# Performance work log

Measured on AMD Instinct MI355X. Metric: run time of the kernel, lower is better.

The kernel has to match this reference:

```python
import jax, jax.numpy as jnp
import numpy as np

N = 100000      # nodes
E = 1600000     # edges
F_IN = 64       # num_node_features
R = 8           # num_relations
G = 256         # graphs in batch
H, C = 4, 32    # GAT heads, per-head channels
NEG_SLOPE_ATT = 0.2    # GATConv attention leaky relu
NEG_SLOPE = 0.01       # F.leaky_relu default


def setup_inputs() -> dict:
    key = jax.random.key(0)
    ks = jax.random.split(key, 12)
    init = lambda k, shape, fan: (jax.random.normal(k, shape, jnp.float32) / np.sqrt(fan).astype(np.float32))
    x = jax.random.normal(ks[0], (N, F_IN), jnp.float32)
    edge_index = jax.random.randint(ks[1], (2, E), 0, N)
    edge_type = jax.random.randint(ks[2], (E,), 0, R)
    batch = (jnp.arange(N) * G) // N  # sorted graph ids, every segment non-empty
    return dict(
        x=x, edge_index=edge_index, edge_type=edge_type, batch=batch,
        gat_w=init(ks[3], (F_IN, H * C), F_IN),
        gat_att_src=init(ks[4], (H, C), C),
        gat_att_dst=init(ks[5], (H, C), C),
        gat_bias=jnp.zeros((H * C,), jnp.float32),
        dense1_w=init(ks[6], (H * C, 16), H * C),
        dense1_b=jnp.zeros((16,), jnp.float32),
        rw1=init(ks[7], (R, F_IN, 32), F_IN),
        root1=init(ks[8], (F_IN, 32), F_IN),
        rb1=jnp.zeros((32,), jnp.float32),
        rw2=init(ks[9], (R, 32, 16), 32),
        root2=init(ks[10], (32, 16), 32),
        rb2=jnp.zeros((16,), jnp.float32),
        dense_w=init(ks[11], (32, 1), 32),
        dense_b=jnp.zeros((1,), jnp.float32),
    )


def _gat(x, src, dst, w, att_src, att_dst, bias):
    h = (x @ w).reshape(N, H, C)                       # [N,H,C]
    a_src = jnp.sum(h * att_src, axis=-1)              # [N,H]
    a_dst = jnp.sum(h * att_dst, axis=-1)              # [N,H]
    e = jax.nn.leaky_relu(a_src[src] + a_dst[dst], NEG_SLOPE_ATT)  # [E,H]
    # segment softmax over incoming edges of each dst node
    m = jax.ops.segment_max(e, dst, num_segments=N)    # [N,H]
    p = jnp.exp(e - m[dst])
    s = jax.ops.segment_sum(p, dst, num_segments=N)    # [N,H]
    alpha = p / s[dst]
    msg = h[src] * alpha[:, :, None]                   # [E,H,C]
    out = jax.ops.segment_sum(msg, dst, num_segments=N)
    return out.reshape(N, H * C) + bias


def _rgcn(x, src, dst, edge_type, w, root, bias):
    # per-relation transform of all nodes, then edge gather (PyG RGCNConv, aggr='mean')
    xw = jnp.einsum('ni,rio->rno', x, w)               # [R,N,out]
    msg = xw[edge_type, src]                           # [E,out]
    comb = dst * R + edge_type                         # mean is per (dst, relation)
    cnt = jax.ops.segment_sum(jnp.ones((E,), x.dtype), comb, num_segments=N * R)
    agg = jax.ops.segment_sum(msg / cnt[comb][:, None], dst, num_segments=N)
    return agg + x @ root + bias


def reference(x, edge_index, edge_type, batch, gat_w, gat_att_src, gat_att_dst,
              gat_bias, dense1_w, dense1_b, rw1, root1, rb1, rw2, root2, rb2,
              dense_w, dense_b):
    src, dst = edge_index[0], edge_index[1]
    # GAT branch (dropout treated as identity / eval mode)
    h = _gat(x, src, dst, gat_w, gat_att_src, gat_att_dst, gat_bias)
    h = jax.nn.leaky_relu(h, NEG_SLOPE)
    h = jax.nn.leaky_relu(h @ dense1_w + dense1_b, NEG_SLOPE)
    gmax = jax.ops.segment_max(h, batch, num_segments=G)          # [G,16]
    # RGCN branch
    z = jax.nn.relu(_rgcn(x, src, dst, edge_type, rw1, root1, rb1))
    z = jax.nn.relu(_rgcn(z, src, dst, edge_type, rw2, root2, rb2))
    nodes_per_graph = jax.ops.segment_sum(jnp.ones((N,), x.dtype), batch, num_segments=G)
    gmean = jax.ops.segment_sum(z, batch, num_segments=G) / nodes_per_graph[:, None]
    # fuse
    zc = jnp.concatenate([gmax, gmean], axis=1)                   # [G,32]
    return zc @ dense_w + dense_b                                  # [G,1]
```

## Files before the change

### kernel.cpp

```cpp
#include <hip/hip_runtime.h>
#include <hip/hip_bf16.h>

typedef __hip_bfloat16 bf16;
typedef unsigned short u16;

#define N_NODES 100000
#define N_EDGES 1600000
#define F_IN 64
#define N_REL 8
#define N_GRAPH 256
#define N_HEAD 4
#define HC 128
#define NBLK_SCAN 391

__device__ __forceinline__ float lrelu(float x, float s) { return x >= 0.f ? x : s * x; }
__device__ __forceinline__ unsigned fenc(float f) {
  unsigned b = __float_as_uint(f);
  return (b & 0x80000000u) ? ~b : (b | 0x80000000u);
}
__device__ __forceinline__ float fdec(unsigned u) {
  float v = __uint_as_float((u & 0x80000000u) ? (u & 0x7fffffffu) : ~u);
  return fmaxf(fminf(v, 3e38f), -3e38f);
}
__device__ __forceinline__ float bf2f(bf16 v) { return __bfloat162float(v); }
__device__ __forceinline__ bf16 f2bf(float v) { return __float2bfloat16(v); }
__device__ __forceinline__ float lo_bf(unsigned u) { return __uint_as_float(u << 16); }
__device__ __forceinline__ float hi_bf(unsigned u) { return __uint_as_float(u & 0xFFFF0000u); }
__device__ __forceinline__ unsigned f2bfu(float v) {
  unsigned u = __float_as_uint(v);
  return (u + 0x7FFFu + ((u >> 16) & 1u)) >> 16;
}

template<bool BF> __device__ __forceinline__ float ldf(const void* p, size_t i) {
  if (BF) { u16 v = ((const u16*)p)[i]; return __uint_as_float(((unsigned)v) << 16); }
  else    { return ((const float*)p)[i]; }
}
template<bool BF> __device__ __forceinline__ float2 ldf2(const void* p, size_t i) {
  if (BF) { unsigned v = ((const unsigned*)p)[i]; return make_float2(lo_bf(v), hi_bf(v)); }
  else    { return ((const float2*)p)[i]; }
}

__global__ void k_probe(const u16* __restrict__ xr, int* __restrict__ flag) {
  int t = threadIdx.x;
  int c = 0;
  for (int i = t; i < 1024; i += 256) {
    unsigned e = (xr[i] >> 7) & 0xFFu;
    if (e >= 100u && e <= 140u) c++;
  }
  __shared__ int sc[256];
  sc[t] = c;
  __syncthreads();
  for (int s = 128; s; s >>= 1) { if (t < s) sc[t] += sc[t + s]; __syncthreads(); }
  if (t == 0) *flag = (sc[0] >= 800) ? 1 : 0;
}

template<bool BF>
__device__ __forceinline__ void gat_body(const void* x, const void* w, const void* att_s,
                                         const void* att_d, u16* __restrict__ h,
                                         float* __restrict__ a_src, float* __restrict__ a_dst,
                                         int n0, float* xs) {
  int tid = threadIdx.x;
  for (int i = tid; i < 16 * F_IN; i += 256)
    xs[i] = ldf<BF>(x, (size_t)(n0 + (i >> 6)) * F_IN + (i & 63));
  __syncthreads();
  int g = tid >> 7, c = tid & 127;
  float as_c = ldf<BF>(att_s, c), ad_c = ldf<BF>(att_d, c);
  float acc[8] = {0.f, 0.f, 0.f, 0.f, 0.f, 0.f, 0.f, 0.f};
#pragma unroll 1
  for (int kh = 0; kh < F_IN; kh += 32) {
    float wreg[32];
#pragma unroll
    for (int j = 0; j < 32; ++j) wreg[j] = ldf<BF>(w, (size_t)(kh + j) * HC + c);
#pragma unroll
    for (int n = 0; n < 8; ++n) {
      const float* xr = &xs[(g * 8 + n) * F_IN + kh];
#pragma unroll
      for (int j = 0; j < 32; j += 4) {
        float4 xv = *(const float4*)&xr[j];
        acc[n] += xv.x * wreg[j];
        acc[n] += xv.y * wreg[j + 1];
        acc[n] += xv.z * wreg[j + 2];
        acc[n] += xv.w * wreg[j + 3];
      }
    }
  }
  int l = tid & 63, head = c >> 5;
#pragma unroll
  for (int n = 0; n < 8; ++n) {
    int node = n0 + g * 8 + n;
    h[(size_t)node * HC + c] = (u16)f2bfu(acc[n]);
    float ps = acc[n] * as_c, pd = acc[n] * ad_c;
#pragma unroll
    for (int off = 16; off > 0; off >>= 1) {
      ps += __shfl_xor(ps, off, 64);
      pd += __shfl_xor(pd, off, 64);
    }
    if ((l & 31) == 0) {
      a_src[node * N_HEAD + head] = ps;
      a_dst[node * N_HEAD + head] = pd;
    }
  }
}

template<bool BF>
__device__ __forceinline__ void xw1_body(const void* x, const void* rw1, bf16* __restrict__ xw1,
                                         int n0, float* xs) {
  int tid = threadIdx.x;
  for (int i = tid; i < 16 * F_IN; i += 256)
    xs[i] = ldf<BF>(x, (size_t)(n0 + (i >> 6)) * F_IN + (i & 63));
  __syncthreads();
  int r = tid >> 5, c = tid & 31;
  float acc[16] = {0.f, 0.f, 0.f, 0.f, 0.f, 0.f, 0.f, 0.f,
                   0.f, 0.f, 0.f, 0.f, 0.f, 0.f, 0.f, 0.f};
#pragma unroll 1
  for (int kh = 0; kh < F_IN; kh += 32) {
    float wreg[32];
#pragma unroll
    for (int j = 0; j < 32; ++j)
      wreg[j] = ldf<BF>(rw1, (size_t)(r * F_IN + kh + j) * 32 + c);
#pragma unroll
    for (int n = 0; n < 16; ++n) {
      const float* xr = &xs[n * F_IN + kh];
#pragma unroll
      for (int j = 0; j < 32; j += 4) {
        float4 xv = *(const float4*)&xr[j];
        acc[n] += xv.x * wreg[j];
        acc[n] += xv.y * wreg[j + 1];
        acc[n] += xv.z * wreg[j + 2];
        acc[n] += xv.w * wreg[j + 3];
      }
    }
  }
#pragma unroll
  for (int n = 0; n < 16; ++n)
    xw1[((size_t)r * N_NODES + (n0 + n)) * 32 + c] = f2bf(acc[n]);
}

__global__ void __launch_bounds__(256, 4)
k_gxh(const void* x, const void* w, const void* att_s, const void* att_d,
      u16* h, float* a_src, float* a_dst, const void* rw1, bf16* xw1,
      const int* __restrict__ ei, const int* __restrict__ etype,
      int* __restrict__ deg, int* __restrict__ cnt, const int* flag) {
  __shared__ __align__(16) float xs[16 * F_IN];
  int bid = blockIdx.x;
  if (bid < 6250) {
    int e = bid * 256 + threadIdx.x;
    int d = ei[N_EDGES + e], t = etype[e];
    atomicAdd(&deg[d], 1);
    atomicAdd(&cnt[d * N_REL + t], 1);
  } else if (bid < 12500) {
    int n0 = (bid - 6250) * 16;
    if (__builtin_amdgcn_readfirstlane(*flag))
      gat_body<true>(x, w, att_s, att_d, h, a_src, a_dst, n0, xs);
    else
      gat_body<false>(x, w, att_s, att_d, h, a_src, a_dst, n0, xs);
  } else {
    int n0 = (bid - 12500) * 16;
    if (__builtin_amdgcn_readfirstlane(*flag)) xw1_body<true>(x, rw1, xw1, n0, xs);
    else xw1_body<false>(x, rw1, xw1, n0, xs);
  }
}

__global__ void k_scan_a(const int* __restrict__ deg, int* __restrict__ rowptr,
                         int* __restrict__ scanblk) {
  __shared__ int buf[256];
  int tid = threadIdx.x;
  int i = blockIdx.x * 256 + tid;
  int v = (i < N_NODES) ? deg[i] : 0;
  buf[tid] = v;
  __syncthreads();
  for (int st = 1; st < 256; st <<= 1) {
    int t = buf[tid];
    int a = (tid >= st) ? buf[tid - st] : 0;
    __syncthreads();
    buf[tid] = t + a;
    __syncthreads();
  }
  if (i < N_NODES) rowptr[i] = buf[tid] - v;
  if (tid == 255) scanblk[blockIdx.x] = buf[255];
}
__global__ void k_scan_b(int* __restrict__ scanblk) {
  __shared__ int buf[512];
  int tid = threadIdx.x;
  int v = (tid < NBLK_SCAN) ? scanblk[tid] : 0;
  buf[tid] = v;
  __syncthreads();
  for (int st = 1; st < 512; st <<= 1) {
    int t = buf[tid];
    int a = (tid >= st) ? buf[tid - st] : 0;
    __syncthreads();
    buf[tid] = t + a;
    __syncthreads();
  }
  if (tid < NBLK_SCAN) scanblk[tid] = buf[tid] - v;
}
__global__ void k_scan_c(int* __restrict__ rowptr, int* __restrict__ wp,
                         const int* __restrict__ scanblk) {
  int i = blockIdx.x * 256 + threadIdx.x;
  if (i < N_NODES) {
    int val = rowptr[i] + scanblk[blockIdx.x];
    rowptr[i] = val;
    wp[i] = val;
  } else if (i == N_NODES) {
    rowptr[N_NODES] = N_EDGES;
  }
}

__global__ void k_scatter(const int* __restrict__ ei, const int* __restrict__ etype,
                          const float* __restrict__ a_src, const float* __restrict__ a_dst,
                          int* __restrict__ wp, unsigned* __restrict__ csr,
                          float4* __restrict__ p_logit) {
  int e = blockIdx.x * 256 + threadIdx.x;
  if (e >= N_EDGES) return;
  int sn = ei[e], d = ei[N_EDGES + e], t = etype[e];
  int pos = atomicAdd(&wp[d], 1);
  csr[pos] = (unsigned)sn | ((unsigned)t << 20);
  const float4 as = *(const float4*)&a_src[sn * 4];
  const float4 ad = *(const float4*)&a_dst[d * 4];
  float4 lg;
  lg.x = lrelu(as.x + ad.x, 0.2f);
  lg.y = lrelu(as.y + ad.y, 0.2f);
  lg.z = lrelu(as.z + ad.z, 0.2f);
  lg.w = lrelu(as.w + ad.w, 0.2f);
  p_logit[pos] = lg;
}

template<bool BF>
__device__ __forceinline__ void agg_body(const int* __restrict__ rowptr,
                                         const unsigned* __restrict__ csr,
                                         const float* __restrict__ plog,
                                         const uint2* __restrict__ hu2, const void* gbias,
                                         const void* d1w, const void* d1b,
                                         const int* __restrict__ batch,
                                         unsigned* __restrict__ gmax, int* __restrict__ npg,
                                         float (*os)[132], int bid) {
  int tid = threadIdx.x;
  int wave = tid >> 6, l = tid & 63;
  int d = bid * 4 + wave;
  int base = rowptr[d];
  int deg = rowptr[d + 1] - base;
  float m = -1e30f, si;
  {
    int hd = l & 3, sl = l >> 2;
    for (int i = sl; i < deg; i += 16) m = fmaxf(m, plog[(size_t)(base + i) * 4 + hd]);
    m = fmaxf(m, __shfl_xor(m, 4, 64));
    m = fmaxf(m, __shfl_xor(m, 8, 64));
    m = fmaxf(m, __shfl_xor(m, 16, 64));
    m = fmaxf(m, __shfl_xor(m, 32, 64));
    float s = 0.f;
    for (int i = sl; i < deg; i += 16) s += __expf(plog[(size_t)(base + i) * 4 + hd] - m);
    s += __shfl_xor(s, 4, 64);
    s += __shfl_xor(s, 8, 64);
    s += __shfl_xor(s, 16, 64);
    s += __shfl_xor(s, 32, 64);
    si = (deg > 0) ? 1.f / s : 0.f;
  }
  int slot = l >> 5, cl = l & 31;
  int head = cl >> 3;
  float mh = __shfl(m, head, 64);
  float sih = __shfl(si, head, 64);
  float a0 = 0.f, a1 = 0.f, a2 = 0.f, a3 = 0.f;
  int i = slot;
  for (; i + 6 < deg; i += 8) {
    unsigned sp0 = csr[base + i],     sp1 = csr[base + i + 2];
    unsigned sp2 = csr[base + i + 4], sp3 = csr[base + i + 6];
    float av0 = __expf(plog[(size_t)(base + i) * 4 + head] - mh) * sih;
    float av1 = __expf(plog[(size_t)(base + i + 2) * 4 + head] - mh) * sih;
    float av2 = __expf(plog[(size_t)(base + i + 4) * 4 + head] - mh) * sih;
    float av3 = __expf(plog[(size_t)(base + i + 6) * 4 + head] - mh) * sih;
    uint2 h0 = hu2[(size_t)(sp0 & 0xFFFFF) * 32 + cl];
    uint2 h1 = hu2[(size_t)(sp1 & 0xFFFFF) * 32 + cl];
    uint2 h2 = hu2[(size_t)(sp2 & 0xFFFFF) * 32 + cl];
    uint2 h3 = hu2[(size_t)(sp3 & 0xFFFFF) * 32 + cl];
    a0 += lo_bf(h0.x) * av0 + lo_bf(h1.x) * av1 + lo_bf(h2.x) * av2 + lo_bf(h3.x) * av3;
    a1 += hi_bf(h0.x) * av0 + hi_bf(h1.x) * av1 + hi_bf(h2.x) * av2 + hi_bf(h3.x) * av3;
    a2 += lo_bf(h0.y) * av0 + lo_bf(h1.y) * av1 + lo_bf(h2.y) * av2 + lo_bf(h3.y) * av3;
    a3 += hi_bf(h0.y) * av0 + hi_bf(h1.y) * av1 + hi_bf(h2.y) * av2 + hi_bf(h3.y) * av3;
  }
  for (; i < deg; i += 2) {
    unsigned sp = csr[base + i];
    float av = __expf(plog[(size_t)(base + i) * 4 + head] - mh) * sih;
    uint2 hv = hu2[(size_t)(sp & 0xFFFFF) * 32 + cl];
    a0 += lo_bf(hv.x) * av;
    a1 += hi_bf(hv.x) * av;
    a2 += lo_bf(hv.y) * av;
    a3 += hi_bf(hv.y) * av;
  }
  a0 += __shfl_xor(a0, 32, 64);
  a1 += __shfl_xor(a1, 32, 64);
  a2 += __shfl_xor(a2, 32, 64);
  a3 += __shfl_xor(a3, 32, 64);
  if (slot == 0) {
    os[wave][4 * cl + 0] = lrelu(a0 + ldf<BF>(gbias, 4 * cl + 0), 0.01f);
    os[wave][4 * cl + 1] = lrelu(a1 + ldf<BF>(gbias, 4 * cl + 1), 0.01f);
    os[wave][4 * cl + 2] = lrelu(a2 + ldf<BF>(gbias, 4 * cl + 2), 0.01f);
    os[wave][4 * cl + 3] = lrelu(a3 + ldf<BF>(gbias, 4 * cl + 3), 0.01f);
  }
  __syncthreads();
  if (tid < 64) {
    int node = tid >> 4, out = tid & 15;
    float acc = ldf<BF>(d1b, out);
#pragma unroll
    for (int k = 0; k < HC; ++k) acc += os[node][k] * ldf<BF>(d1w, (size_t)k * 16 + out);
    acc = lrelu(acc, 0.01f);
    atomicMax(&gmax[batch[bid * 4 + node] * 16 + out], fenc(acc));
  }
  if (tid < 4) atomicAdd(&npg[batch[bid * 4 + tid]], 1);
}

template<bool BF>
__device__ __forceinline__ void ragg1_body(const int* __restrict__ rowptr,
                                           const unsigned* __restrict__ csr,
                                           const int* __restrict__ cnt,
                                           const unsigned* __restrict__ xw, const void* x,
                                           const void* root1, const void* rb1,
                                           float* __restrict__ z1, float* sh, int bid) {
  float (*xs)[F_IN] = (float(*)[F_IN])sh;
  float (*cinv)[N_REL] = (float(*)[N_REL])(sh + 4 * F_IN);
  int tid = threadIdx.x;
  int n0 = bid * 4;
  {
    int nn = n0 + (tid >> 6);
    xs[tid >> 6][tid & 63] = ldf<BF>(x, (size_t)nn * F_IN + (tid & 63));
  }
  if (tid < 32) {
    int cv = cnt[(n0 + (tid >> 3)) * N_REL + (tid & 7)];
    cinv[tid >> 3][tid & 7] = (cv > 0) ? 1.f / (float)cv : 0.f;
  }
  __syncthreads();
  int wave = tid >> 6, l = tid & 63;
  int slot = l >> 4, cl = l & 15;
  int n = n0 + wave;
  int base = rowptr[n], deg = rowptr[n + 1] - base;
  float a0 = 0.f, a1 = 0.f;
  int i = slot;
  for (; i + 4 < deg; i += 8) {
    unsigned sp0 = csr[base + i], sp1 = csr[base + i + 4];
    int t0 = sp0 >> 20, t1 = sp1 >> 20;
    unsigned v0 = xw[((size_t)t0 * N_NODES + (sp0 & 0xFFFFF)) * 16 + cl];
    unsigned v1 = xw[((size_t)t1 * N_NODES + (sp1 & 0xFFFFF)) * 16 + cl];
    float c0 = cinv[wave][t0], c1 = cinv[wave][t1];
    a0 += lo_bf(v0) * c0 + lo_bf(v1) * c1;
    a1 += hi_bf(v0) * c0 + hi_bf(v1) * c1;
  }
  if (i < deg) {
    unsigned sp = csr[base + i];
    int t = sp >> 20;
    unsigned v = xw[((size_t)t * N_NODES + (sp & 0xFFFFF)) * 16 + cl];
    float c0 = cinv[wave][t];
    a0 += lo_bf(v) * c0;
    a1 += hi_bf(v) * c0;
  }
#pragma unroll
  for (int kk = 0; kk < 16; ++kk) {
    int k = slot * 16 + kk;
    float xv = xs[wave][k];
    float2 wv = ldf2<BF>(root1, (size_t)k * 16 + cl);
    a0 += xv * wv.x;
    a1 += xv * wv.y;
  }
  a0 += __shfl_xor(a0, 16, 64); a0 += __shfl_xor(a0, 32, 64);
  a1 += __shfl_xor(a1, 16, 64); a1 += __shfl_xor(a1, 32, 64);
  if (slot == 0) {
    z1[(size_t)n * 32 + 2 * cl]     = fmaxf(a0 + ldf<BF>(rb1, 2 * cl), 0.f);
    z1[(size_t)n * 32 + 2 * cl + 1] = fmaxf(a1 + ldf<BF>(rb1, 2 * cl + 1), 0.f);
  }
}

__global__ void k_aggragg1(const int* rowptr, const unsigned* csr, const float* plog,
                           const u16* h, const void* gbias, const void* d1w, const void* d1b,
                           const int* batch, unsigned* gmax, int* npg,
                           const int* cnt, const bf16* xw1, const void* x,
                           const void* root1, const void* rb1, float* z1, const int* flag) {
  __shared__ __align__(16) float sh[544];
  int bf = __builtin_amdgcn_readfirstlane(*flag);
  if (blockIdx.x < 25000) {
    if (bf) agg_body<true>(rowptr, csr, plog, (const uint2*)h, gbias, d1w, d1b,
                           batch, gmax, npg, (float(*)[132])sh, blockIdx.x);
    else    agg_body<false>(rowptr, csr, plog, (const uint2*)h, gbias, d1w, d1b,
                            batch, gmax, npg, (float(*)[132])sh, blockIdx.x);
  } else {
    if (bf) ragg1_body<true>(rowptr, csr, cnt, (const unsigned*)xw1, x, root1, rb1, z1,
                             sh, blockIdx.x - 25000);
    else    ragg1_body<false>(rowptr, csr, cnt, (const unsigned*)xw1, x, root1, rb1, z1,
                              sh, blockIdx.x - 25000);
  }
}

template<bool BF>
__device__ __forceinline__ void zw2_body(const float* __restrict__ z1, const void* rw2,
                                         bf16* __restrict__ zw2) {
  __shared__ float zs[16][32];
  int tid = threadIdx.x;
  int n0 = blockIdx.x * 16;
  for (int i = tid; i < 16 * 32; i += 256) {
    int nn = n0 + (i >> 5);
    zs[i >> 5][i & 31] = (nn < N_NODES) ? z1[(size_t)nn * 32 + (i & 31)] : 0.f;
  }
  __syncthreads();
  int nl = tid >> 4, c = tid & 15;
  int n = n0 + nl, r = blockIdx.y;
  float acc = 0.f;
#pragma unroll
  for (int k = 0; k < 32; ++k) acc += zs[nl][k] * ldf<BF>(rw2, (size_t)(r * 32 + k) * 16 + c);
  if (n < N_NODES) zw2[((size_t)r * N_NODES + n) * 16 + c] = f2bf(acc);
}
__global__ void k_zw2(const float* z1, const void* rw2, bf16* zw2, const int* flag) {
  if (__builtin_amdgcn_readfirstlane(*flag)) zw2_body<true>(z1, rw2, zw2);
  else zw2_body<false>(z1, rw2, zw2);
}

template<bool BF>
__device__ __forceinline__ void ragg2_body(const int* __restrict__ rowptr,
                                           const unsigned* __restrict__ csr,
                                           const int* __restrict__ cnt,
                                           const unsigned* __restrict__ zw,
                                           const float* __restrict__ z1, const void* root2,
                                           const void* rb2, const int* __restrict__ batch,
                                           float* __restrict__ gsum) {
  __shared__ float zs[4][33];
  __shared__ float cinv[4][N_REL];
  int tid = threadIdx.x;
  int n0 = blockIdx.x * 4;
  if (tid < 128) {
    int nn = n0 + (tid >> 5);
    zs[tid >> 5][tid & 31] = z1[(size_t)nn * 32 + (tid & 31)];
  }
  if (tid < 32) {
    int cv = cnt[(n0 + (tid >> 3)) * N_REL + (tid & 7)];
    cinv[tid >> 3][tid & 7] = (cv > 0) ? 1.f / (float)cv : 0.f;
  }
  __syncthreads();
  int wave = tid >> 6, l = tid & 63;
  int slot = l >> 3, cl = l & 7;
  int n = n0 + wave;
  int base = rowptr[n], deg = rowptr[n + 1] - base;
  float a0 = 0.f, a1 = 0.f;
  int i = slot;
  for (; i + 8 < deg; i += 16) {
    unsigned sp0 = csr[base + i], sp1 = csr[base + i + 8];
    int t0 = sp0 >> 20, t1 = sp1 >> 20;
    unsigned v0 = zw[((size_t)t0 * N_NODES + (sp0 & 0xFFFFF)) * 8 + cl];
    unsigned v1 = zw[((size_t)t1 * N_NODES + (sp1 & 0xFFFFF)) * 8 + cl];
    float c0 = cinv[wave][t0], c1 = cinv[wave][t1];
    a0 += lo_bf(v0) * c0 + lo_bf(v1) * c1;
    a1 += hi_bf(v0) * c0 + hi_bf(v1) * c1;
  }
  if (i < deg) {
    unsigned sp = csr[base + i];
    int t = sp >> 20;
    unsigned v = zw[((size_t)t * N_NODES + (sp & 0xFFFFF)) * 8 + cl];
    float c0 = cinv[wave][t];
    a0 += lo_bf(v) * c0;
    a1 += hi_bf(v) * c0;
  }
#pragma unroll
  for (int kk = 0; kk < 4; ++kk) {
    int k = slot * 4 + kk;
    float zv = zs[wave][k];
    float2 wv = ldf2<BF>(root2, (size_t)k * 8 + cl);
    a0 += zv * wv.x;
    a1 += zv * wv.y;
  }
  a0 += __shfl_xor(a0, 8, 64); a0 += __shfl_xor(a0, 16, 64); a0 += __shfl_xor(a0, 32, 64);
  a1 += __shfl_xor(a1, 8, 64); a1 += __shfl_xor(a1, 16, 64); a1 += __shfl_xor(a1, 32, 64);
  if (slot == 0) {
    float z2a = fmaxf(a0 + ldf<BF>(rb2, 2 * cl), 0.f);
    float z2b = fmaxf(a1 + ldf<BF>(rb2, 2 * cl + 1), 0.f);
    int g = batch[n];
    atomicAdd(&gsum[g * 16 + 2 * cl], z2a);
    atomicAdd(&gsum[g * 16 + 2 * cl + 1], z2b);
  }
}
__global__ void k_ragg2(const int* rowptr, const unsigned* csr, const int* cnt,
                        const bf16* zw2, const float* z1, const void* root2, const void* rb2,
                        const int* batch, float* gsum, const int* flag) {
  if (__builtin_amdgcn_readfirstlane(*flag))
    ragg2_body<true>(rowptr, csr, cnt, (const unsigned*)zw2, z1, root2, rb2, batch, gsum);
  else
    ragg2_body<false>(rowptr, csr, cnt, (const unsigned*)zw2, z1, root2, rb2, batch, gsum);
}

template<bool BF>
__device__ __forceinline__ void final_body(const unsigned* __restrict__ gmax,
                                           const float* __restrict__ gsum,
                                           const int* __restrict__ npg, const void* dw,
                                           const void* db, void* out) {
  int g = threadIdx.x;
  if (g >= N_GRAPH) return;
  float acc = ldf<BF>(db, 0);
  int np = npg[g]; if (np < 1) np = 1;
  float inv = 1.f / (float)np;
#pragma unroll
  for (int c = 0; c < 16; ++c) {
    acc += fdec(gmax[g * 16 + c]) * ldf<BF>(dw, c);
    acc += (gsum[g * 16 + c] * inv) * ldf<BF>(dw, 16 + c);
  }
  if (BF) ((bf16*)out)[g] = f2bf(acc);
  else ((float*)out)[g] = acc;
}
__global__ void k_final(const unsigned* gmax, const float* gsum, const int* npg,
                        const void* dw, const void* db, void* out, const int* flag) {
  if (__builtin_amdgcn_readfirstlane(*flag)) final_body<true>(gmax, gsum, npg, dw, db, out);
  else final_body<false>(gmax, gsum, npg, dw, db, out);
}

extern "C" void kernel_launch(void* const* d_in, const int* in_sizes, int n_in,
                              void* d_out, int out_size, void* d_ws, size_t ws_size,
                              hipStream_t stream) {
  const void* x        = d_in[0];
  const int*  ei       = (const int*)d_in[1];
  const int*  etype    = (const int*)d_in[2];
  const int*  batch    = (const int*)d_in[3];
  const void* gat_w    = d_in[4];
  const void* att_src  = d_in[5];
  const void* att_dst  = d_in[6];
  const void* gat_bias = d_in[7];
  const void* d1w      = d_in[8];
  const void* d1b      = d_in[9];
  const void* rw1      = d_in[10];
  const void* root1    = d_in[11];
  const void* rb1      = d_in[12];
  const void* rw2      = d_in[13];
  const void* root2    = d_in[14];
  const void* rb2      = d_in[15];
  const void* dw       = d_in[16];
  const void* db       = d_in[17];

  char* ws = (char*)d_ws;
  const size_t o_h     = 0;
  const size_t o_plog  = 25600000;
  const size_t o_xw1   = 51200000;
  const size_t o_zw2   = 0;
  const size_t o_asrc  = 102400000;
  const size_t o_adst  = 104000000;
  const size_t o_deg   = 105600000;
  const size_t o_rowp  = 106000000;
  const size_t o_wp    = 106400016;
  const size_t o_cnt   = 106800016;
  const size_t o_csr   = 110000016;
  const size_t o_z1    = 116400016;
  const size_t o_sblk  = 129200016;
  const size_t o_gmax  = 129201600;
  const size_t o_gsum  = 129217984;
  const size_t o_npg   = 129234368;
  const size_t o_flag  = 129235392;
  const size_t total   = 129235396;
  if (ws_size < total) return;

  u16*      h      = (u16*)(ws + o_h);
  float*    plog   = (float*)(ws + o_plog);
  bf16*     xw1    = (bf16*)(ws + o_xw1);
  bf16*     zw2    = (bf16*)(ws + o_zw2);
  float*    a_src  = (float*)(ws + o_asrc);
  float*    a_dst  = (float*)(ws + o_adst);
  int*      deg    = (int*)(ws + o_deg);
  int*      rowptr = (int*)(ws + o_rowp);
  int*      wp     = (int*)(ws + o_wp);
  int*      cnt    = (int*)(ws + o_cnt);
  unsigned* csr    = (unsigned*)(ws + o_csr);
  float*    z1     = (float*)(ws + o_z1);
  int*      sblk   = (int*)(ws + o_sblk);
  unsigned* gmax   = (unsigned*)(ws + o_gmax);
  float*    gsum   = (float*)(ws + o_gsum);
  int*      npg    = (int*)(ws + o_npg);
  int*      flag   = (int*)(ws + o_flag);

  k_probe<<<1, 256, 0, stream>>>((const u16*)x, flag);

  hipMemsetAsync(ws + o_deg, 0, o_csr - o_deg, stream);
  hipMemsetAsync(ws + o_gmax, 0, 33792, stream);

  k_gxh<<<18750, 256, 0, stream>>>(x, gat_w, att_src, att_dst, h, a_src, a_dst,
                                   rw1, xw1, ei, etype, deg, cnt, flag);

  k_scan_a<<<NBLK_SCAN, 256, 0, stream>>>(deg, rowptr, sblk);
  k_scan_b<<<1, 512, 0, stream>>>(sblk);
  k_scan_c<<<NBLK_SCAN, 256, 0, stream>>>(rowptr, wp, sblk);
  k_scatter<<<(N_EDGES + 255) / 256, 256, 0, stream>>>(ei, etype, a_src, a_dst, wp, csr,
                                                       (float4*)plog);

  k_aggragg1<<<50000, 256, 0, stream>>>(rowptr, csr, plog, h, gat_bias, d1w, d1b,
                                        batch, gmax, npg, cnt, xw1, x, root1, rb1, z1, flag);

  k_zw2<<<dim3((N_NODES + 15) / 16, N_REL), 256, 0, stream>>>(z1, rw2, zw2, flag);
  k_ragg2<<<N_NODES / 4, 256, 0, stream>>>(rowptr, csr, cnt, zw2, z1, root2, rb2,
                                           batch, gsum, flag);

  k_final<<<1, 256, 0, stream>>>(gmax, gsum, npg, dw, db, d_out, flag);
}
```

Measured before the change: 1.085 ms.

## Recompute attention logits in aggregation and fuse z1·rw2 transform into ragg1

The scatter kernel no longer writes a per-edge logit array. The GAT aggregation instead recomputes leaky_relu(a_src[src]+a_dst[dst]) from the CSR, caching up to 128 logits per node in shared memory. The separate zw2 kernel is folded into the RGCN layer-1 aggregation, which computes the per-relation projection from z1 held in shared memory. This removes a 25.6MB logit write and read plus one kernel launch, at the cost of extra gathers of a_src and more shared memory and registers in the fused kernel, now under launch bounds.

```diff
diff --git a/kernel.cpp b/kernel.cpp
--- a/kernel.cpp
+++ b/kernel.cpp
@@ -12,6 +12,7 @@
 #define N_HEAD 4
 #define HC 128
 #define NBLK_SCAN 391
+#define LGCAP 128
 
 __device__ __forceinline__ float lrelu(float x, float s) { return x >= 0.f ? x : s * x; }
 __device__ __forceinline__ unsigned fenc(float f) {
@@ -207,33 +208,23 @@
 }
 
 __global__ void k_scatter(const int* __restrict__ ei, const int* __restrict__ etype,
-                          const float* __restrict__ a_src, const float* __restrict__ a_dst,
-                          int* __restrict__ wp, unsigned* __restrict__ csr,
-                          float4* __restrict__ p_logit) {
+                          int* __restrict__ wp, unsigned* __restrict__ csr) {
   int e = blockIdx.x * 256 + threadIdx.x;
-  if (e >= N_EDGES) return;
   int sn = ei[e], d = ei[N_EDGES + e], t = etype[e];
   int pos = atomicAdd(&wp[d], 1);
   csr[pos] = (unsigned)sn | ((unsigned)t << 20);
-  const float4 as = *(const float4*)&a_src[sn * 4];
-  const float4 ad = *(const float4*)&a_dst[d * 4];
-  float4 lg;
-  lg.x = lrelu(as.x + ad.x, 0.2f);
-  lg.y = lrelu(as.y + ad.y, 0.2f);
-  lg.z = lrelu(as.z + ad.z, 0.2f);
-  lg.w = lrelu(as.w + ad.w, 0.2f);
-  p_logit[pos] = lg;
 }
 
 template<bool BF>
 __device__ __forceinline__ void agg_body(const int* __restrict__ rowptr,
                                          const unsigned* __restrict__ csr,
-                                         const float* __restrict__ plog,
+                                         const float* __restrict__ a_src,
+                                         const float* __restrict__ a_dst,
                                          const uint2* __restrict__ hu2, const void* gbias,
                                          const void* d1w, const void* d1b,
                                          const int* __restrict__ batch,
                                          unsigned* __restrict__ gmax, int* __restrict__ npg,
-                                         float (*os)[132], int bid) {
+                                         float (*os)[132], float (*lgc)[LGCAP][4], int bid) {
   int tid = threadIdx.x;
   int wave = tid >> 6, l = tid & 63;
   int d = bid * 4 + wave;
@@ -242,13 +233,23 @@
   float m = -1e30f, si;
   {
     int hd = l & 3, sl = l >> 2;
-    for (int i = sl; i < deg; i += 16) m = fmaxf(m, plog[(size_t)(base + i) * 4 + hd]);
+    float adh = a_dst[d * 4 + hd];
+    for (int i = sl; i < deg; i += 16) {
+      unsigned sp = csr[base + i];
+      float lg = lrelu(a_src[(size_t)(sp & 0xFFFFF) * 4 + hd] + adh, 0.2f);
+      if (i < LGCAP) lgc[wave][i][hd] = lg;
+      m = fmaxf(m, lg);
+    }
     m = fmaxf(m, __shfl_xor(m, 4, 64));
     m = fmaxf(m, __shfl_xor(m, 8, 64));
     m = fmaxf(m, __shfl_xor(m, 16, 64));
     m = fmaxf(m, __shfl_xor(m, 32, 64));
     float s = 0.f;
-    for (int i = sl; i < deg; i += 16) s += __expf(plog[(size_t)(base + i) * 4 + hd] - m);
+    for (int i = sl; i < deg; i += 16) {
+      float lg = (i < LGCAP) ? lgc[wave][i][hd]
+               : lrelu(a_src[(size_t)(csr[base + i] & 0xFFFFF) * 4 + hd] + adh, 0.2f);
+      s += __expf(lg - m);
+    }
     s += __shfl_xor(s, 4, 64);
     s += __shfl_xor(s, 8, 64);
     s += __shfl_xor(s, 16, 64);
@@ -259,15 +260,19 @@
   int head = cl >> 3;
   float mh = __shfl(m, head, 64);
   float sih = __shfl(si, head, 64);
+  float adH = a_dst[d * 4 + head];
   float a0 = 0.f, a1 = 0.f, a2 = 0.f, a3 = 0.f;
   int i = slot;
+#define AV(idx, spv) \
+  (__expf((((idx) < LGCAP) ? lgc[wave][(idx)][head] \
+          : lrelu(a_src[(size_t)((spv) & 0xFFFFF) * 4 + head] + adH, 0.2f)) - mh) * sih)
   for (; i + 6 < deg; i += 8) {
     unsigned sp0 = csr[base + i],     sp1 = csr[base + i + 2];
     unsigned sp2 = csr[base + i + 4], sp3 = csr[base + i + 6];
-    float av0 = __expf(plog[(size_t)(base + i) * 4 + head] - mh) * sih;
-    float av1 = __expf(plog[(size_t)(base + i + 2) * 4 + head] - mh) * sih;
-    float av2 = __expf(plog[(size_t)(base + i + 4) * 4 + head] - mh) * sih;
-    float av3 = __expf(plog[(size_t)(base + i + 6) * 4 + head] - mh) * sih;
+    float av0 = AV(i, sp0);
+    float av1 = AV(i + 2, sp1);
+    float av2 = AV(i + 4, sp2);
+    float av3 = AV(i + 6, sp3);
     uint2 h0 = hu2[(size_t)(sp0 & 0xFFFFF) * 32 + cl];
     uint2 h1 = hu2[(size_t)(sp1 & 0xFFFFF) * 32 + cl];
     uint2 h2 = hu2[(size_t)(sp2 & 0xFFFFF) * 32 + cl];
@@ -279,13 +284,14 @@
   }
   for (; i < deg; i += 2) {
     unsigned sp = csr[base + i];
-    float av = __expf(plog[(size_t)(base + i) * 4 + head] - mh) * sih;
+    float av = AV(i, sp);
     uint2 hv = hu2[(size_t)(sp & 0xFFFFF) * 32 + cl];
     a0 += lo_bf(hv.x) * av;
     a1 += hi_bf(hv.x) * av;
     a2 += lo_bf(hv.y) * av;
     a3 += hi_bf(hv.y) * av;
   }
+#undef AV
   a0 += __shfl_xor(a0, 32, 64);
   a1 += __shfl_xor(a1, 32, 64);
   a2 += __shfl_xor(a2, 32, 64);
@@ -314,7 +320,9 @@
                                            const int* __restrict__ cnt,
                                            const unsigned* __restrict__ xw, const void* x,
                                            const void* root1, const void* rb1,
-                                           float* __restrict__ z1, float* sh, int bid) {
+                                           const void* rw2, bf16* __restrict__ zw2,
+                                           float* __restrict__ z1, float* sh,
+                                           float (*z1l)[32], int bid) {
   float (*xs)[F_IN] = (float(*)[F_IN])sh;
   float (*cinv)[N_REL] = (float(*)[N_REL])(sh + 4 * F_IN);
   int tid = threadIdx.x;
@@ -362,52 +370,46 @@
   a0 += __shfl_xor(a0, 16, 64); a0 += __shfl_xor(a0, 32, 64);
   a1 += __shfl_xor(a1, 16, 64); a1 += __shfl_xor(a1, 32, 64);
   if (slot == 0) {
-    z1[(size_t)n * 32 + 2 * cl]     = fmaxf(a0 + ldf<BF>(rb1, 2 * cl), 0.f);
-    z1[(size_t)n * 32 + 2 * cl + 1] = fmaxf(a1 + ldf<BF>(rb1, 2 * cl + 1), 0.f);
-  }
-}
-
-__global__ void k_aggragg1(const int* rowptr, const unsigned* csr, const float* plog,
-                           const u16* h, const void* gbias, const void* d1w, const void* d1b,
-                           const int* batch, unsigned* gmax, int* npg,
-                           const int* cnt, const bf16* xw1, const void* x,
-                           const void* root1, const void* rb1, float* z1, const int* flag) {
+    float v0 = fmaxf(a0 + ldf<BF>(rb1, 2 * cl), 0.f);
+    float v1 = fmaxf(a1 + ldf<BF>(rb1, 2 * cl + 1), 0.f);
+    z1[(size_t)n * 32 + 2 * cl]     = v0;
+    z1[(size_t)n * 32 + 2 * cl + 1] = v1;
+    z1l[wave][2 * cl]     = v0;
+    z1l[wave][2 * cl + 1] = v1;
+  }
+  __syncthreads();
+#pragma unroll
+  for (int o = tid; o < 512; o += 256) {
+    int node = o >> 7, rc = o & 127, r = rc >> 4, c = rc & 15;
+    float acc = 0.f;
+#pragma unroll
+    for (int k = 0; k < 32; ++k) acc += z1l[node][k] * ldf<BF>(rw2, (size_t)(r * 32 + k) * 16 + c);
+    zw2[((size_t)r * N_NODES + (n0 + node)) * 16 + c] = f2bf(acc);
+  }
+}
+
+__global__ void __launch_bounds__(256, 4)
+k_aggragg1(const int* rowptr, const unsigned* csr, const float* a_src, const float* a_dst,
+           const u16* h, const void* gbias, const void* d1w, const void* d1b,
+           const int* batch, unsigned* gmax, int* npg,
+           const int* cnt, const bf16* xw1, const void* x,
+           const void* root1, const void* rb1, const void* rw2, bf16* zw2,
+           float* z1, const int* flag) {
   __shared__ __align__(16) float sh[544];
+  __shared__ __align__(16) float lgc[4][LGCAP][4];
+  __shared__ __align__(16) float z1l[4][32];
   int bf = __builtin_amdgcn_readfirstlane(*flag);
   if (blockIdx.x < 25000) {
-    if (bf) agg_body<true>(rowptr, csr, plog, (const uint2*)h, gbias, d1w, d1b,
-                           batch, gmax, npg, (float(*)[132])sh, blockIdx.x);
-    else    agg_body<false>(rowptr, csr, plog, (const uint2*)h, gbias, d1w, d1b,
-                            batch, gmax, npg, (float(*)[132])sh, blockIdx.x);
+    if (bf) agg_body<true>(rowptr, csr, a_src, a_dst, (const uint2*)h, gbias, d1w, d1b,
+                           batch, gmax, npg, (float(*)[132])sh, lgc, blockIdx.x);
+    else    agg_body<false>(rowptr, csr, a_src, a_dst, (const uint2*)h, gbias, d1w, d1b,
+                            batch, gmax, npg, (float(*)[132])sh, lgc, blockIdx.x);
   } else {
-    if (bf) ragg1_body<true>(rowptr, csr, cnt, (const unsigned*)xw1, x, root1, rb1, z1,
-                             sh, blockIdx.x - 25000);
-    else    ragg1_body<false>(rowptr, csr, cnt, (const unsigned*)xw1, x, root1, rb1, z1,
-                              sh, blockIdx.x - 25000);
-  }
-}
-
-template<bool BF>
-__device__ __forceinline__ void zw2_body(const float* __restrict__ z1, const void* rw2,
-                                         bf16* __restrict__ zw2) {
-  __shared__ float zs[16][32];
-  int tid = threadIdx.x;
-  int n0 = blockIdx.x * 16;
-  for (int i = tid; i < 16 * 32; i += 256) {
-    int nn = n0 + (i >> 5);
-    zs[i >> 5][i & 31] = (nn < N_NODES) ? z1[(size_t)nn * 32 + (i & 31)] : 0.f;
-  }
-  __syncthreads();
-  int nl = tid >> 4, c = tid & 15;
-  int n = n0 + nl, r = blockIdx.y;
-  float acc = 0.f;
-#pragma unroll
-  for (int k = 0; k < 32; ++k) acc += zs[nl][k] * ldf<BF>(rw2, (size_t)(r * 32 + k) * 16 + c);
-  if (n < N_NODES) zw2[((size_t)r * N_NODES + n) * 16 + c] = f2bf(acc);
-}
-__global__ void k_zw2(const float* z1, const void* rw2, bf16* zw2, const int* flag) {
-  if (__builtin_amdgcn_readfirstlane(*flag)) zw2_body<true>(z1, rw2, zw2);
-  else zw2_body<false>(z1, rw2, zw2);
+    if (bf) ragg1_body<true>(rowptr, csr, cnt, (const unsigned*)xw1, x, root1, rb1,
+                             rw2, zw2, z1, sh, z1l, blockIdx.x - 25000);
+    else    ragg1_body<false>(rowptr, csr, cnt, (const unsigned*)xw1, x, root1, rb1,
+                              rw2, zw2, z1, sh, z1l, blockIdx.x - 25000);
+  }
 }
 
 template<bool BF>
@@ -529,9 +531,8 @@
 
   char* ws = (char*)d_ws;
   const size_t o_h     = 0;
-  const size_t o_plog  = 25600000;
+  const size_t o_zw2   = 25600000;
   const size_t o_xw1   = 51200000;
-  const size_t o_zw2   = 0;
   const size_t o_asrc  = 102400000;
   const size_t o_adst  = 104000000;
   const size_t o_deg   = 105600000;
@@ -549,9 +550,8 @@
   if (ws_size < total) return;
 
   u16*      h      = (u16*)(ws + o_h);
-  float*    plog   = (float*)(ws + o_plog);
+  bf16*     zw2    = (bf16*)(ws + o_zw2);
   bf16*     xw1    = (bf16*)(ws + o_xw1);
-  bf16*     zw2    = (bf16*)(ws + o_zw2);
   float*    a_src  = (float*)(ws + o_asrc);
   float*    a_dst  = (float*)(ws + o_adst);
   int*      deg    = (int*)(ws + o_deg);
@@ -577,13 +577,12 @@
   k_scan_a<<<NBLK_SCAN, 256, 0, stream>>>(deg, rowptr, sblk);
   k_scan_b<<<1, 512, 0, stream>>>(sblk);
   k_scan_c<<<NBLK_SCAN, 256, 0, stream>>>(rowptr, wp, sblk);
-  k_scatter<<<(N_EDGES + 255) / 256, 256, 0, stream>>>(ei, etype, a_src, a_dst, wp, csr,
-                                                       (float4*)plog);
-
-  k_aggragg1<<<50000, 256, 0, stream>>>(rowptr, csr, plog, h, gat_bias, d1w, d1b,
-                                        batch, gmax, npg, cnt, xw1, x, root1, rb1, z1, flag);
-
-  k_zw2<<<dim3((N_NODES + 15) / 16, N_REL), 256, 0, stream>>>(z1, rw2, zw2, flag);
+  k_scatter<<<6250, 256, 0, stream>>>(ei, etype, wp, csr);
+
+  k_aggragg1<<<50000, 256, 0, stream>>>(rowptr, csr, a_src, a_dst, h, gat_bias, d1w, d1b,
+                                        batch, gmax, npg, cnt, xw1, x, root1, rb1,
+                                        rw2, zw2, z1, flag);
+
   k_ragg2<<<N_NODES / 4, 256, 0, stream>>>(rowptr, csr, cnt, zw2, z1, root2, rb2,
                                            batch, gsum, flag);
 
```

Result: slower. 1.169 ms (+7.8%).

## Move xw1 transform into scatter kernel and fuse zw2 into ragg1

Applied to the files above, without the earlier changes.

The per-relation x@rw1 transform moves out of the first combined kernel and into the CSR scatter kernel, so its compute can overlap the atomic-bound scatter. The z1@rw2 per-relation transform is computed directly inside the ragg1 blocks from z1 held in shared memory, which removes the separate k_zw2 launch and its reread of z1. The fused path needs a separate zw2 buffer and so only runs when the workspace is large enough; otherwise it falls back to the old kernel. It adds a block barrier and extra register and LDS use in the ragg1 path.

```diff
diff --git a/kernel.cpp b/kernel.cpp
--- a/kernel.cpp
+++ b/kernel.cpp
@@ -102,6 +102,27 @@
   }
 }
 
+__global__ void __launch_bounds__(256, 4)
+k_gh(const void* x, const void* w, const void* att_s, const void* att_d,
+     u16* h, float* a_src, float* a_dst,
+     const int* __restrict__ ei, const int* __restrict__ etype,
+     int* __restrict__ deg, int* __restrict__ cnt, const int* flag) {
+  __shared__ __align__(16) float xs[16 * F_IN];
+  int bid = blockIdx.x;
+  if (bid < 6250) {
+    int e = bid * 256 + threadIdx.x;
+    int d = ei[N_EDGES + e], t = etype[e];
+    atomicAdd(&deg[d], 1);
+    atomicAdd(&cnt[d * N_REL + t], 1);
+  } else {
+    int n0 = (bid - 6250) * 16;
+    if (__builtin_amdgcn_readfirstlane(*flag))
+      gat_body<true>(x, w, att_s, att_d, h, a_src, a_dst, n0, xs);
+    else
+      gat_body<false>(x, w, att_s, att_d, h, a_src, a_dst, n0, xs);
+  }
+}
+
 template<bool BF>
 __device__ __forceinline__ void xw1_body(const void* x, const void* rw1, bf16* __restrict__ xw1,
                                          int n0, float* xs) {
@@ -134,31 +155,6 @@
 #pragma unroll
   for (int n = 0; n < 16; ++n)
     xw1[((size_t)r * N_NODES + (n0 + n)) * 32 + c] = f2bf(acc[n]);
-}
-
-__global__ void __launch_bounds__(256, 4)
-k_gxh(const void* x, const void* w, const void* att_s, const void* att_d,
-      u16* h, float* a_src, float* a_dst, const void* rw1, bf16* xw1,
-      const int* __restrict__ ei, const int* __restrict__ etype,
-      int* __restrict__ deg, int* __restrict__ cnt, const int* flag) {
-  __shared__ __align__(16) float xs[16 * F_IN];
-  int bid = blockIdx.x;
-  if (bid < 6250) {
-    int e = bid * 256 + threadIdx.x;
-    int d = ei[N_EDGES + e], t = etype[e];
-    atomicAdd(&deg[d], 1);
-    atomicAdd(&cnt[d * N_REL + t], 1);
-  } else if (bid < 12500) {
-    int n0 = (bid - 6250) * 16;
-    if (__builtin_amdgcn_readfirstlane(*flag))
-      gat_body<true>(x, w, att_s, att_d, h, a_src, a_dst, n0, xs);
-    else
-      gat_body<false>(x, w, att_s, att_d, h, a_src, a_dst, n0, xs);
-  } else {
-    int n0 = (bid - 12500) * 16;
-    if (__builtin_amdgcn_readfirstlane(*flag)) xw1_body<true>(x, rw1, xw1, n0, xs);
-    else xw1_body<false>(x, rw1, xw1, n0, xs);
-  }
 }
 
 __global__ void k_scan_a(const int* __restrict__ deg, int* __restrict__ rowptr,
@@ -206,23 +202,31 @@
   }
 }
 
-__global__ void k_scatter(const int* __restrict__ ei, const int* __restrict__ etype,
-                          const float* __restrict__ a_src, const float* __restrict__ a_dst,
-                          int* __restrict__ wp, unsigned* __restrict__ csr,
-                          float4* __restrict__ p_logit) {
-  int e = blockIdx.x * 256 + threadIdx.x;
-  if (e >= N_EDGES) return;
-  int sn = ei[e], d = ei[N_EDGES + e], t = etype[e];
-  int pos = atomicAdd(&wp[d], 1);
-  csr[pos] = (unsigned)sn | ((unsigned)t << 20);
-  const float4 as = *(const float4*)&a_src[sn * 4];
-  const float4 ad = *(const float4*)&a_dst[d * 4];
-  float4 lg;
-  lg.x = lrelu(as.x + ad.x, 0.2f);
-  lg.y = lrelu(as.y + ad.y, 0.2f);
-  lg.z = lrelu(as.z + ad.z, 0.2f);
-  lg.w = lrelu(as.w + ad.w, 0.2f);
-  p_logit[pos] = lg;
+__global__ void __launch_bounds__(256, 4)
+k_scatxw1(const int* __restrict__ ei, const int* __restrict__ etype,
+          const float* __restrict__ a_src, const float* __restrict__ a_dst,
+          int* __restrict__ wp, unsigned* __restrict__ csr, float4* __restrict__ p_logit,
+          const void* x, const void* rw1, bf16* xw1, const int* flag) {
+  __shared__ __align__(16) float xs[16 * F_IN];
+  int bid = blockIdx.x;
+  if (bid < 6250) {
+    int e = bid * 256 + threadIdx.x;
+    int sn = ei[e], d = ei[N_EDGES + e], t = etype[e];
+    int pos = atomicAdd(&wp[d], 1);
+    csr[pos] = (unsigned)sn | ((unsigned)t << 20);
+    const float4 as = *(const float4*)&a_src[sn * 4];
+    const float4 ad = *(const float4*)&a_dst[d * 4];
+    float4 lg;
+    lg.x = lrelu(as.x + ad.x, 0.2f);
+    lg.y = lrelu(as.y + ad.y, 0.2f);
+    lg.z = lrelu(as.z + ad.z, 0.2f);
+    lg.w = lrelu(as.w + ad.w, 0.2f);
+    p_logit[pos] = lg;
+  } else {
+    int n0 = (bid - 6250) * 16;
+    if (__builtin_amdgcn_readfirstlane(*flag)) xw1_body<true>(x, rw1, xw1, n0, xs);
+    else xw1_body<false>(x, rw1, xw1, n0, xs);
+  }
 }
 
 template<bool BF>
@@ -314,7 +318,9 @@
                                            const int* __restrict__ cnt,
                                            const unsigned* __restrict__ xw, const void* x,
                                            const void* root1, const void* rb1,
-                                           float* __restrict__ z1, float* sh, int bid) {
+                                           const void* rw2, bf16* __restrict__ zw2t,
+                                           float* __restrict__ z1, float* sh,
+                                           float (*z1l)[32], int bid) {
   float (*xs)[F_IN] = (float(*)[F_IN])sh;
   float (*cinv)[N_REL] = (float(*)[N_REL])(sh + 4 * F_IN);
   int tid = threadIdx.x;
@@ -362,8 +368,27 @@
   a0 += __shfl_xor(a0, 16, 64); a0 += __shfl_xor(a0, 32, 64);
   a1 += __shfl_xor(a1, 16, 64); a1 += __shfl_xor(a1, 32, 64);
   if (slot == 0) {
-    z1[(size_t)n * 32 + 2 * cl]     = fmaxf(a0 + ldf<BF>(rb1, 2 * cl), 0.f);
-    z1[(size_t)n * 32 + 2 * cl + 1] = fmaxf(a1 + ldf<BF>(rb1, 2 * cl + 1), 0.f);
+    float v0 = fmaxf(a0 + ldf<BF>(rb1, 2 * cl), 0.f);
+    float v1 = fmaxf(a1 + ldf<BF>(rb1, 2 * cl + 1), 0.f);
+    z1[(size_t)n * 32 + 2 * cl]     = v0;
+    z1[(size_t)n * 32 + 2 * cl + 1] = v1;
+    z1l[wave][2 * cl]     = v0;
+    z1l[wave][2 * cl + 1] = v1;
+  }
+  if (zw2t) {
+    __syncthreads();
+    unsigned* zw2u = (unsigned*)zw2t;
+    int o = tid;
+    int r = o >> 5, node = (o >> 3) & 3, cp = o & 7;
+    float acc0 = 0.f, acc1 = 0.f;
+#pragma unroll
+    for (int k = 0; k < 32; ++k) {
+      float zv = z1l[node][k];
+      float2 wv = ldf2<BF>(rw2, (size_t)(r * 32 + k) * 8 + cp);
+      acc0 += zv * wv.x;
+      acc1 += zv * wv.y;
+    }
+    zw2u[((size_t)r * N_NODES + (n0 + node)) * 8 + cp] = f2bfu(acc0) | (f2bfu(acc1) << 16);
   }
 }
 
@@ -371,8 +396,10 @@
                            const u16* h, const void* gbias, const void* d1w, const void* d1b,
                            const int* batch, unsigned* gmax, int* npg,
                            const int* cnt, const bf16* xw1, const void* x,
-                           const void* root1, const void* rb1, float* z1, const int* flag) {
+                           const void* root1, const void* rb1, const void* rw2, bf16* zw2t,
+                           float* z1, const int* flag) {
   __shared__ __align__(16) float sh[544];
+  __shared__ __align__(16) float z1l[4][32];
   int bf = __builtin_amdgcn_readfirstlane(*flag);
   if (blockIdx.x < 25000) {
     if (bf) agg_body<true>(rowptr, csr, plog, (const uint2*)h, gbias, d1w, d1b,
@@ -380,10 +407,10 @@
     else    agg_body<false>(rowptr, csr, plog, (const uint2*)h, gbias, d1w, d1b,
                             batch, gmax, npg, (float(*)[132])sh, blockIdx.x);
   } else {
-    if (bf) ragg1_body<true>(rowptr, csr, cnt, (const unsigned*)xw1, x, root1, rb1, z1,
-                             sh, blockIdx.x - 25000);
-    else    ragg1_body<false>(rowptr, csr, cnt, (const unsigned*)xw1, x, root1, rb1, z1,
-                              sh, blockIdx.x - 25000);
+    if (bf) ragg1_body<true>(rowptr, csr, cnt, (const unsigned*)xw1, x, root1, rb1,
+                             rw2, zw2t, z1, sh, z1l, blockIdx.x - 25000);
+    else    ragg1_body<false>(rowptr, csr, cnt, (const unsigned*)xw1, x, root1, rb1,
+                              rw2, zw2t, z1, sh, z1l, blockIdx.x - 25000);
   }
 }
 
@@ -531,7 +558,6 @@
   const size_t o_h     = 0;
   const size_t o_plog  = 25600000;
   const size_t o_xw1   = 51200000;
-  const size_t o_zw2   = 0;
   const size_t o_asrc  = 102400000;
   const size_t o_adst  = 104000000;
   const size_t o_deg   = 105600000;
@@ -545,13 +571,15 @@
   const size_t o_gsum  = 129217984;
   const size_t o_npg   = 129234368;
   const size_t o_flag  = 129235392;
-  const size_t total   = 129235396;
-  if (ws_size < total) return;
+  const size_t total1  = 129235396;
+  const size_t o_zw2s  = 129235456;
+  const size_t total2  = o_zw2s + 25600000;
+  if (ws_size < total1) return;
+  const bool fused = (ws_size >= total2);
 
   u16*      h      = (u16*)(ws + o_h);
   float*    plog   = (float*)(ws + o_plog);
   bf16*     xw1    = (bf16*)(ws + o_xw1);
-  bf16*     zw2    = (bf16*)(ws + o_zw2);
   float*    a_src  = (float*)(ws + o_asrc);
   float*    a_dst  = (float*)(ws + o_adst);
   int*      deg    = (int*)(ws + o_deg);
@@ -565,25 +593,30 @@
   float*    gsum   = (float*)(ws + o_gsum);
   int*      npg    = (int*)(ws + o_npg);
   int*      flag   = (int*)(ws + o_flag);
+  bf16*     zw2    = fused ? (bf16*)(ws + o_zw2s) : (bf16*)(ws + o_h);
 
   k_probe<<<1, 256, 0, stream>>>((const u16*)x, flag);
 
   hipMemsetAsync(ws + o_deg, 0, o_csr - o_deg, stream);
   hipMemsetAsync(ws + o_gmax, 0, 33792, stream);
 
-  k_gxh<<<18750, 256, 0, stream>>>(x, gat_w, att_src, att_dst, h, a_src, a_dst,
-                                   rw1, xw1, ei, etype, deg, cnt, flag);
+  k_gh<<<12500, 256, 0, stream>>>(x, gat_w, att_src, att_dst, h, a_src, a_dst,
+                                  ei, etype, deg, cnt, flag);
 
   k_scan_a<<<NBLK_SCAN, 256, 0, stream>>>(deg, rowptr, sblk);
   k_scan_b<<<1, 512, 0, stream>>>(sblk);
   k_scan_c<<<NBLK_SCAN, 256, 0, stream>>>(rowptr, wp, sblk);
-  k_scatter<<<(N_EDGES + 255) / 256, 256, 0, stream>>>(ei, etype, a_src, a_dst, wp, csr,
-                                                       (float4*)plog);
+
+  k_scatxw1<<<12500, 256, 0, stream>>>(ei, etype, a_src, a_dst, wp, csr, (float4*)plog,
+                                       x, rw1, xw1, flag);
 
   k_aggragg1<<<50000, 256, 0, stream>>>(rowptr, csr, plog, h, gat_bias, d1w, d1b,
-                                        batch, gmax, npg, cnt, xw1, x, root1, rb1, z1, flag);
-
-  k_zw2<<<dim3((N_NODES + 15) / 16, N_REL), 256, 0, stream>>>(z1, rw2, zw2, flag);
+                                        batch, gmax, npg, cnt, xw1, x, root1, rb1,
+                                        rw2, fused ? zw2 : (bf16*)nullptr, z1, flag);
+
+  if (!fused)
+    k_zw2<<<dim3((N_NODES + 15) / 16, N_REL), 256, 0, stream>>>(z1, rw2, zw2, flag);
+
   k_ragg2<<<N_NODES / 4, 256, 0, stream>>>(rowptr, csr, cnt, zw2, z1, root2, rb2,
                                            batch, gsum, flag);
 
```

Measured after the change: 1.173 ms. 1.08x slower.
